# Performance work log

Hardware: AMD Instinct MI355X
Metric: run time of the kernel (lower is better)

Reference implementation:

```python
import jax, jax.numpy as jnp
import numpy as np

D_MODEL = 1024
D_HEAD = 64


def setup_inputs() -> dict:
    key = jax.random.key(0)
    k_x, k_q, k_k, k_v, k_o = jax.random.split(key, 5)
    scale = 1.0 / np.sqrt(D_MODEL)
    residual_stream = jax.random.normal(k_x, (4, 2048, D_MODEL), dtype=jnp.float32)
    Q = scale * jax.random.normal(k_q, (D_MODEL, D_HEAD), dtype=jnp.float32)
    K = scale * jax.random.normal(k_k, (D_MODEL, D_HEAD), dtype=jnp.float32)
    V = scale * jax.random.normal(k_v, (D_MODEL, D_HEAD), dtype=jnp.float32)
    O = scale * jax.random.normal(k_o, (D_MODEL, D_HEAD), dtype=jnp.float32)
    return {"residual_stream": residual_stream, "Q": Q, "K": K, "V": V, "O": O}


def reference(residual_stream, Q, K, V, O) -> jnp.ndarray:
    # queries/keys: [B, S, d_head]
    queries = jnp.einsum('bsd,dh->bsh', residual_stream, Q)
    keys = jnp.einsum('bsd,dh->bsh', residual_stream, K)
    # NOTE: original module applies NO 1/sqrt(d_head) scaling.
    pre_attention = jnp.einsum('bqh,bkh->bqk', queries, keys)  # [B, S, S]
    S = pre_attention.shape[-1]
    causal = jnp.tril(jnp.ones((S, S), dtype=bool))
    pre_attention = jnp.where(causal[None], pre_attention, -jnp.inf)
    attention = jax.nn.softmax(pre_attention, axis=-1)
    # x = residual @ V @ O^T : [B, S, d_model]
    x = jnp.einsum('bsd,dh,eh->bse', residual_stream, V, O)
    return jnp.einsum('bqk,bke->bqe', attention, x)
```

## Files before the change

### kernel.cpp

```cpp
#include <hip/hip_runtime.h>
#include <hip/hip_bf16.h>
#include <math.h>

#define BATCH 4
#define SEQ   2048
#define DM    1024
#define DH    64
#define NROWS (BATCH*SEQ)
#define PVSPLIT 8

typedef __hip_bfloat16 bf16;
typedef __attribute__((ext_vector_type(8))) short short8;
typedef __attribute__((ext_vector_type(8))) unsigned short ushortx8;
typedef __attribute__((ext_vector_type(4))) float floatx4;

__device__ __forceinline__ ushort f2bf(float f) {
    union { bf16 h; ushort u; } cv;
    cv.h = __float2bfloat16(f);
    return cv.u;
}
__device__ __forceinline__ float bf2f(ushort u) {
    union { unsigned int i; float f; } v; v.i = ((unsigned int)u) << 16; return v.f;
}

__device__ __forceinline__ void load_lds16(const ushort* g, ushort* l) {
    __builtin_amdgcn_global_load_lds(
        (const __attribute__((address_space(1))) unsigned int*)g,
        (__attribute__((address_space(3))) unsigned int*)l, 16, 0, 0);
}

__global__ __launch_bounds__(256) void wprep_kernel(
    const float* __restrict__ Q, const float* __restrict__ K,
    const float* __restrict__ V, const float* __restrict__ O,
    ushort* __restrict__ WhT, ushort* __restrict__ WlT,
    ushort* __restrict__ Oh, ushort* __restrict__ Ol)
{
    int n = blockIdx.x;
    if (n < 192) {
        const float* W = (n < 64) ? Q : (n < 128) ? K : V;
        int c = n & 63;
        for (int k = threadIdx.x; k < DM; k += 256) {
            float w = W[k * DH + c];
            ushort hi = f2bf(w);
            WhT[n * DM + k] = hi;
            WlT[n * DM + k] = f2bf(w - bf2f(hi));
        }
    } else {
        int e0 = (n - 192) << 4;
        for (int idx = threadIdx.x; idx < 16 * DH; idx += 256) {
            int off = (e0 << 6) + idx;
            float w = O[off];
            ushort hi = f2bf(w);
            Oh[off] = hi;
            Ol[off] = f2bf(w - bf2f(hi));
        }
    }
}

__global__ __launch_bounds__(256) void qkv_part_kernel(
    const float* __restrict__ x, const ushort* __restrict__ WhT,
    const ushort* __restrict__ WlT, float* __restrict__ Cpart)
{
    __shared__ __align__(16) ushort Xs[2][32][34];
    __shared__ __align__(16) ushort Ws[2][192][34];
    int s0 = blockIdx.x * 32;
    int kb = blockIdx.y * 256;
    int t = threadIdx.x;
    int wave = t >> 6, lane = t & 63, m_ = lane & 15, qd = lane >> 4;
    const floatx4 z4 = {0.f, 0.f, 0.f, 0.f};
    floatx4 accq[2] = {z4, z4}, acck[2] = {z4, z4}, accv[2] = {z4, z4};
    int xr = t >> 3, xc = (t & 7) * 4;
    for (int k0 = 0; k0 < 256; k0 += 32) {
        float4 v = *(const float4*)&x[(size_t)(s0 + xr) * DM + kb + k0 + xc];
        ushort h0 = f2bf(v.x), h1 = f2bf(v.y), h2 = f2bf(v.z), h3 = f2bf(v.w);
        *(ushort4*)&Xs[0][xr][xc] = make_ushort4(h0, h1, h2, h3);
        *(ushort4*)&Xs[1][xr][xc] = make_ushort4(
            f2bf(v.x - bf2f(h0)), f2bf(v.y - bf2f(h1)),
            f2bf(v.z - bf2f(h2)), f2bf(v.w - bf2f(h3)));
        #pragma unroll
        for (int j = 0; j < 3; ++j) {
            int idx = t + j * 256, n = idx >> 2, kc = (idx & 3) * 8;
            *(uint4*)&Ws[0][n][kc] = *(const uint4*)&WhT[n * DM + kb + k0 + kc];
            *(uint4*)&Ws[1][n][kc] = *(const uint4*)&WlT[n * DM + kb + k0 + kc];
        }
        __syncthreads();
        short8 ah[2], al[2];
        #pragma unroll
        for (int mi = 0; mi < 2; ++mi) {
            ah[mi] = *(const short8*)&Xs[0][mi * 16 + m_][qd * 8];
            al[mi] = *(const short8*)&Xs[1][mi * 16 + m_][qd * 8];
        }
        int nq = wave * 16 + m_, nk = 64 + wave * 16 + m_, nv = 128 + wave * 16 + m_;
        short8 bqh = *(const short8*)&Ws[0][nq][qd * 8];
        short8 bql = *(const short8*)&Ws[1][nq][qd * 8];
        short8 bkh = *(const short8*)&Ws[0][nk][qd * 8];
        short8 bkl = *(const short8*)&Ws[1][nk][qd * 8];
        short8 bvh = *(const short8*)&Ws[0][nv][qd * 8];
        #pragma unroll
        for (int mi = 0; mi < 2; ++mi) {
            accq[mi] = __builtin_amdgcn_mfma_f32_16x16x32_bf16(ah[mi], bqh, accq[mi], 0, 0, 0);
            accq[mi] = __builtin_amdgcn_mfma_f32_16x16x32_bf16(al[mi], bqh, accq[mi], 0, 0, 0);
            accq[mi] = __builtin_amdgcn_mfma_f32_16x16x32_bf16(ah[mi], bql, accq[mi], 0, 0, 0);
            acck[mi] = __builtin_amdgcn_mfma_f32_16x16x32_bf16(ah[mi], bkh, acck[mi], 0, 0, 0);
            acck[mi] = __builtin_amdgcn_mfma_f32_16x16x32_bf16(al[mi], bkh, acck[mi], 0, 0, 0);
            acck[mi] = __builtin_amdgcn_mfma_f32_16x16x32_bf16(ah[mi], bkl, acck[mi], 0, 0, 0);
            accv[mi] = __builtin_amdgcn_mfma_f32_16x16x32_bf16(ah[mi], bvh, accv[mi], 0, 0, 0);
        }
        __syncthreads();
    }
    float* Cp = Cpart + (size_t)blockIdx.y * (NROWS * 192);
    #pragma unroll
    for (int mi = 0; mi < 2; ++mi) {
        #pragma unroll
        for (int r = 0; r < 4; ++r) {
            int row = s0 + mi * 16 + qd * 4 + r;
            float* base = Cp + (size_t)row * 192;
            base[wave * 16 + m_]       = accq[mi][r];
            base[64 + wave * 16 + m_]  = acck[mi][r];
            base[128 + wave * 16 + m_] = accv[mi][r];
        }
    }
}

__global__ __launch_bounds__(256) void qkv_reduce_kernel(
    const float* __restrict__ Cpart,
    ushort* __restrict__ qh, ushort* __restrict__ ql,
    ushort* __restrict__ kh, ushort* __restrict__ kl, ushort* __restrict__ xvhT)
{
    __shared__ ushort xvs[32][72];
    const size_t SL = (size_t)NROWS * 192;
    int row0 = blockIdx.x * 32;
    int t = threadIdx.x;
    #pragma unroll
    for (int i = 0; i < 24; ++i) {
        int e = i * 256 + t;
        int r = e / 192, c = e - r * 192;
        size_t row = row0 + r;
        size_t off = row * 192 + c;
        float s = Cpart[off] + Cpart[SL + off] + Cpart[2 * SL + off] + Cpart[3 * SL + off];
        ushort hi = f2bf(s);
        if (c < 64) {
            qh[row * 64 + c] = hi; ql[row * 64 + c] = f2bf(s - bf2f(hi));
        } else if (c < 128) {
            kh[row * 64 + c - 64] = hi; kl[row * 64 + c - 64] = f2bf(s - bf2f(hi));
        } else {
            xvs[r][c - 128] = hi;
        }
    }
    __syncthreads();
    int h = t >> 2, seg = t & 3;
    ushortx8 v;
    #pragma unroll
    for (int k = 0; k < 8; ++k) v[k] = xvs[seg * 8 + k][h];
    int b = row0 >> 11, sl = row0 & 2047;
    *(ushortx8*)&xvhT[(((size_t)(b * 64 + h)) << 11) + sl + seg * 8] = v;
}

__global__ __launch_bounds__(256) void softmax_kernel(
    const ushort* __restrict__ qh, const ushort* __restrict__ ql,
    const ushort* __restrict__ kh, const ushort* __restrict__ kl,
    ushort* __restrict__ P, float* __restrict__ lpart)
{
    __shared__ __align__(16) ushort Qs[2][2][32][72];
    __shared__ float lred[4][2][32];
    int pp = blockIdx.x & 31, b = blockIdx.x >> 5, s = blockIdx.y;
    int jA = pp, jB = 63 - pp;
    int srowA = jA << 5, srowB = jB << 5;
    int s0gA = (b << 11) + srowA, s0gB = (b << 11) + srowB;
    int t = threadIdx.x, wave = t >> 6, lane = t & 63, m_ = lane & 15, qd = lane >> 4;
    #pragma unroll
    for (int i = 0; i < 4; ++i) {
        int idx = i * 256 + t;
        int tile = idx >> 9, hl = (idx >> 8) & 1, r = (idx >> 3) & 31, c = (idx & 7) * 8;
        const ushort* src = (hl ? ql : qh) + (size_t)((tile ? s0gB : s0gA) + r) * 64 + c;
        *(uint4*)&Qs[tile][hl][r][c] = *(const uint4*)src;
    }
    __syncthreads();
    const ushort* khb = kh + ((size_t)b << 11) * 64;
    const ushort* klb = kl + ((size_t)b << 11) * 64;
    int ntA = (jA >> 1) + 1, ntB = (jB >> 1) + 1;
    int nAs = (ntA > s) ? (((ntA - 1 - s) >> 2) + 1) : 0;
    int nBs = (ntB > s) ? (((ntB - 1 - s) >> 2) + 1) : 0;
    int ntot = nAs + nBs;
    const floatx4 z4 = {0.f, 0.f, 0.f, 0.f};
    float llA[2][4] = {{0.f,0.f,0.f,0.f},{0.f,0.f,0.f,0.f}};
    float llB[2][4] = {{0.f,0.f,0.f,0.f},{0.f,0.f,0.f,0.f}};
    for (int it = wave; it < ntot; it += 4) {
        int isA = (it < nAs);
        int ti = isA ? (s + 4 * it) : (s + 4 * (it - nAs));
        int srow = isA ? srowA : srowB;
        int s0g = isA ? s0gA : s0gB;
        int tidx = isA ? 0 : 1;
        int k0 = ti << 6;
        floatx4 acc[2][4];
        #pragma unroll
        for (int mi = 0; mi < 2; ++mi)
            #pragma unroll
            for (int ni = 0; ni < 4; ++ni) acc[mi][ni] = z4;
        #pragma unroll
        for (int kk = 0; kk < 2; ++kk) {
            short8 ah0 = *(const short8*)&Qs[tidx][0][0 * 16 + m_][kk * 32 + qd * 8];
            short8 ah1 = *(const short8*)&Qs[tidx][0][1 * 16 + m_][kk * 32 + qd * 8];
            short8 al0 = *(const short8*)&Qs[tidx][1][0 * 16 + m_][kk * 32 + qd * 8];
            short8 al1 = *(const short8*)&Qs[tidx][1][1 * 16 + m_][kk * 32 + qd * 8];
            #pragma unroll
            for (int ni = 0; ni < 4; ++ni) {
                size_t koff = (size_t)(k0 + ni * 16 + m_) * 64 + kk * 32 + qd * 8;
                short8 bh = *(const short8*)&khb[koff];
                short8 bl = *(const short8*)&klb[koff];
                acc[0][ni] = __builtin_amdgcn_mfma_f32_16x16x32_bf16(ah0, bh, acc[0][ni], 0, 0, 0);
                acc[0][ni] = __builtin_amdgcn_mfma_f32_16x16x32_bf16(al0, bh, acc[0][ni], 0, 0, 0);
                acc[0][ni] = __builtin_amdgcn_mfma_f32_16x16x32_bf16(ah0, bl, acc[0][ni], 0, 0, 0);
                acc[1][ni] = __builtin_amdgcn_mfma_f32_16x16x32_bf16(ah1, bh, acc[1][ni], 0, 0, 0);
                acc[1][ni] = __builtin_amdgcn_mfma_f32_16x16x32_bf16(al1, bh, acc[1][ni], 0, 0, 0);
                acc[1][ni] = __builtin_amdgcn_mfma_f32_16x16x32_bf16(ah1, bl, acc[1][ni], 0, 0, 0);
            }
        }
        #pragma unroll
        for (int mi = 0; mi < 2; ++mi)
            #pragma unroll
            for (int ni = 0; ni < 4; ++ni) {
                int kc = k0 + ni * 16 + m_;
                #pragma unroll
                for (int r = 0; r < 4; ++r) {
                    int row = srow + mi * 16 + qd * 4 + r;
                    float p = (kc <= row) ? __expf(acc[mi][ni][r]) : 0.f;
                    if (isA) llA[mi][r] += p; else llB[mi][r] += p;
                    P[(size_t)(s0g + mi * 16 + qd * 4 + r) * 2048 + kc] = f2bf(p);
                }
            }
    }
    #pragma unroll
    for (int d = 1; d < 16; d <<= 1)
        #pragma unroll
        for (int mi = 0; mi < 2; ++mi)
            #pragma unroll
            for (int r = 0; r < 4; ++r) {
                llA[mi][r] += __shfl_xor(llA[mi][r], d);
                llB[mi][r] += __shfl_xor(llB[mi][r], d);
            }
    if (m_ == 0)
        #pragma unroll
        for (int mi = 0; mi < 2; ++mi)
            #pragma unroll
            for (int r = 0; r < 4; ++r) {
                lred[wave][0][mi * 16 + qd * 4 + r] = llA[mi][r];
                lred[wave][1][mi * 16 + qd * 4 + r] = llB[mi][r];
            }
    __syncthreads();
    if (t < 64) {
        int tile = t >> 5, row = t & 31;
        float sm = lred[0][tile][row] + lred[1][tile][row]
                 + lred[2][tile][row] + lred[3][tile][row];
        lpart[(size_t)s * NROWS + (tile ? s0gB : s0gA) + row] = sm;
    }
}

__global__ __launch_bounds__(256) void pv_kernel(
    const ushort* __restrict__ P, const ushort* __restrict__ xvhT,
    float* __restrict__ AxvPart)
{
    __shared__ __align__(16) ushort AL[2][64 * 64];
    __shared__ __align__(16) ushort AS[2][64 * 64];
    __shared__ __align__(16) ushort Bs[2][64 * 64];
    int bid = blockIdx.x;
    int p = bid >> 5;
    int b = (bid >> 3) & 3;
    int s = bid & 7;
    int m0L = (31 - p) << 6, m0S = p << 6;
    int ntL = 32 - p, ntS = p + 1;
    int nL = (ntL - s + 7) >> 3;
    int nS = (ntS > s) ? ((ntS - s + 7) >> 3) : 0;
    int t = threadIdx.x, wave = t >> 6, lane = t & 63, m_ = lane & 15, qd = lane >> 4;
    const ushort* Pb = P + ((size_t)b << 22);
    const ushort* Xb = xvhT + ((size_t)(b * 64) << 11);
    const floatx4 z4 = {0.f, 0.f, 0.f, 0.f};
    floatx4 accL[2][2], accS[2][2];
    #pragma unroll
    for (int mi = 0; mi < 2; ++mi)
        #pragma unroll
        for (int ni = 0; ni < 2; ++ni) { accL[mi][ni] = z4; accS[mi][ni] = z4; }
    int mb = (wave >> 1) << 5;
    int nb = (wave & 1) << 5;
    int drow = lane >> 3;
    int dlc = ((lane & 7) ^ drow) << 3;
    #define PV_STAGE(tt, buf)                                                    \
        {                                                                        \
            int k0_ = (s + 8 * (tt)) << 6;                                       \
            _Pragma("unroll")                                                    \
            for (int i_ = 0; i_ < 6; ++i_) {                                     \
                int c_ = wave * 6 + i_;                                          \
                if (c_ < 8)                                                      \
                    load_lds16(Pb + (size_t)(m0L + c_ * 8 + drow) * SEQ + k0_ + dlc, \
                               &AL[buf][c_ * 512]);                              \
                else if (c_ < 16)                                                \
                    load_lds16(Xb + (size_t)((c_ - 8) * 8 + drow) * SEQ + k0_ + dlc, \
                               &Bs[buf][(c_ - 8) * 512]);                        \
                else if ((tt) < nS)                                              \
                    load_lds16(Pb + (size_t)(m0S + (c_ - 16) * 8 + drow) * SEQ + k0_ + dlc, \
                               &AS[buf][(c_ - 16) * 512]);                       \
            }                                                                    \
        }
    PV_STAGE(0, 0)
    for (int tt = 0; tt < nL; ++tt) {
        __syncthreads();
        if (tt + 1 < nL) PV_STAGE(tt + 1, (tt + 1) & 1)
        int bufi = tt & 1;
        #pragma unroll
        for (int kk = 0; kk < 2; ++kk) {
            short8 bb[2];
            #pragma unroll
            for (int ni = 0; ni < 2; ++ni) {
                int row = nb + ni * 16 + m_;
                bb[ni] = *(const short8*)&Bs[bufi][row * 64 + (((kk << 2) + qd) ^ (row & 7)) * 8];
            }
            #pragma unroll
            for (int mi = 0; mi < 2; ++mi) {
                int row = mb + mi * 16 + m_;
                short8 aL = *(const short8*)&AL[bufi][row * 64 + (((kk << 2) + qd) ^ (row & 7)) * 8];
                #pragma unroll
                for (int ni = 0; ni < 2; ++ni)
                    accL[mi][ni] = __builtin_amdgcn_mfma_f32_16x16x32_bf16(aL, bb[ni], accL[mi][ni], 0, 0, 0);
            }
            if (tt < nS) {
                #pragma unroll
                for (int mi = 0; mi < 2; ++mi) {
                    int row = mb + mi * 16 + m_;
                    short8 aS = *(const short8*)&AS[bufi][row * 64 + (((kk << 2) + qd) ^ (row & 7)) * 8];
                    #pragma unroll
                    for (int ni = 0; ni < 2; ++ni)
                        accS[mi][ni] = __builtin_amdgcn_mfma_f32_16x16x32_bf16(aS, bb[ni], accS[mi][ni], 0, 0, 0);
                }
            }
        }
    }
    float* Ap = AxvPart + (size_t)s * (NROWS * DH);
    #pragma unroll
    for (int mi = 0; mi < 2; ++mi) {
        #pragma unroll
        for (int r = 0; r < 4; ++r) {
            int rowL = m0L + mb + mi * 16 + qd * 4 + r;
            int rowS = m0S + mb + mi * 16 + qd * 4 + r;
            float* orL = Ap + (size_t)((b << 11) + rowL) * DH + nb;
            float* orS = Ap + (size_t)((b << 11) + rowS) * DH + nb;
            #pragma unroll
            for (int ni = 0; ni < 2; ++ni) {
                orL[ni * 16 + m_] = accL[mi][ni][r];
                orS[ni * 16 + m_] = accS[mi][ni][r];
            }
        }
    }
    #undef PV_STAGE
}

__global__ __launch_bounds__(256) void axv_reduce_kernel(
    const float* __restrict__ AxvPart, const float* __restrict__ lpart,
    ushort* __restrict__ Axvh, ushort* __restrict__ Axvl)
{
    const size_t PSL = (size_t)NROWS * DH;
    int idx = blockIdx.x * 256 + threadIdx.x;
    size_t e = (size_t)idx * 4;
    int r = (int)(e >> 6);
    float4 a = *(const float4*)&AxvPart[e];
    #pragma unroll
    for (int sp = 1; sp < PVSPLIT; ++sp) {
        float4 v = *(const float4*)&AxvPart[sp * PSL + e];
        a.x += v.x; a.y += v.y; a.z += v.z; a.w += v.w;
    }
    float sc = 1.f / (lpart[r] + lpart[NROWS + r]
                    + lpart[2 * NROWS + r] + lpart[3 * NROWS + r]);
    a.x *= sc; a.y *= sc; a.z *= sc; a.w *= sc;
    ushort h0 = f2bf(a.x), h1 = f2bf(a.y), h2 = f2bf(a.z), h3 = f2bf(a.w);
    *(ushort4*)&Axvh[e] = make_ushort4(h0, h1, h2, h3);
    *(ushort4*)&Axvl[e] = make_ushort4(
        f2bf(a.x - bf2f(h0)), f2bf(a.y - bf2f(h1)),
        f2bf(a.z - bf2f(h2)), f2bf(a.w - bf2f(h3)));
}

__global__ __launch_bounds__(256) void out_kernel(
    const ushort* __restrict__ Axvh, const ushort* __restrict__ Axvl,
    const ushort* __restrict__ Oh, const ushort* __restrict__ Ol,
    float* __restrict__ out)
{
    __shared__ __align__(16) ushort As[2][64][72];
    __shared__ __align__(16) ushort Bsh[2][128][72];
    int bid = blockIdx.x;
    int r0 = (bid >> 3) << 6;
    int e0 = (bid & 7) << 7;
    int t = threadIdx.x;
    {
        int tr = t >> 2, tc = (t & 3) << 4;
        const ushort* ah = Axvh + (size_t)(r0 + tr) * DH + tc;
        const ushort* al = Axvl + (size_t)(r0 + tr) * DH + tc;
        *(uint4*)&As[0][tr][tc]     = *(const uint4*)ah;
        *(uint4*)&As[0][tr][tc + 8] = *(const uint4*)(ah + 8);
        *(uint4*)&As[1][tr][tc]     = *(const uint4*)al;
        *(uint4*)&As[1][tr][tc + 8] = *(const uint4*)(al + 8);
    }
    {
        int tr = t >> 1, tc = (t & 1) << 5;
        const ushort* bh = Oh + (size_t)(e0 + tr) * DH + tc;
        const ushort* bl = Ol + (size_t)(e0 + tr) * DH + tc;
        *(uint4*)&Bsh[0][tr][tc]      = *(const uint4*)bh;
        *(uint4*)&Bsh[0][tr][tc + 8]  = *(const uint4*)(bh + 8);
        *(uint4*)&Bsh[0][tr][tc + 16] = *(const uint4*)(bh + 16);
        *(uint4*)&Bsh[0][tr][tc + 24] = *(const uint4*)(bh + 24);
        *(uint4*)&Bsh[1][tr][tc]      = *(const uint4*)bl;
        *(uint4*)&Bsh[1][tr][tc + 8]  = *(const uint4*)(bl + 8);
        *(uint4*)&Bsh[1][tr][tc + 16] = *(const uint4*)(bl + 16);
        *(uint4*)&Bsh[1][tr][tc + 24] = *(const uint4*)(bl + 24);
    }
    __syncthreads();
    int wave = t >> 6, lane = t & 63, m_ = lane & 15, qd = lane >> 4;
    const floatx4 z4 = {0.f, 0.f, 0.f, 0.f};
    floatx4 acc[8] = {z4, z4, z4, z4, z4, z4, z4, z4};
    #pragma unroll
    for (int kk = 0; kk < 2; ++kk) {
        short8 ah = *(const short8*)&As[0][wave * 16 + m_][kk * 32 + qd * 8];
        short8 al = *(const short8*)&As[1][wave * 16 + m_][kk * 32 + qd * 8];
        #pragma unroll
        for (int ni = 0; ni < 8; ++ni) {
            short8 bh = *(const short8*)&Bsh[0][ni * 16 + m_][kk * 32 + qd * 8];
            short8 bl = *(const short8*)&Bsh[1][ni * 16 + m_][kk * 32 + qd * 8];
            acc[ni] = __builtin_amdgcn_mfma_f32_16x16x32_bf16(ah, bh, acc[ni], 0, 0, 0);
            acc[ni] = __builtin_amdgcn_mfma_f32_16x16x32_bf16(al, bh, acc[ni], 0, 0, 0);
            acc[ni] = __builtin_amdgcn_mfma_f32_16x16x32_bf16(ah, bl, acc[ni], 0, 0, 0);
        }
    }
    #pragma unroll
    for (int r = 0; r < 4; ++r) {
        int row = r0 + wave * 16 + qd * 4 + r;
        float* orow = out + (size_t)row * DM + e0;
        #pragma unroll
        for (int ni = 0; ni < 8; ++ni)
            orow[ni * 16 + m_] = acc[ni][r];
    }
}

extern "C" void kernel_launch(void* const* d_in, const int* in_sizes, int n_in,
                              void* d_out, int out_size, void* d_ws, size_t ws_size,
                              hipStream_t stream) {
    const float* x = (const float*)d_in[0];
    const float* Q = (const float*)d_in[1];
    const float* K = (const float*)d_in[2];
    const float* V = (const float*)d_in[3];
    const float* O = (const float*)d_in[4];
    float* out = (float*)d_out;

    char* ws = (char*)d_ws;
    ushort* qh   = (ushort*)(ws);
    ushort* ql   = (ushort*)(ws + (1ull  << 20));
    ushort* kh   = (ushort*)(ws + (2ull  << 20));
    ushort* kl   = (ushort*)(ws + (3ull  << 20));
    ushort* xvhT = (ushort*)(ws + (4ull  << 20));
    ushort* WhT  = (ushort*)(ws + (5ull  << 20));
    ushort* WlT  = (ushort*)(ws + (5ull  << 20) + (512ull << 10));
    float*  lpart = (float*)(ws + (6ull  << 20));
    ushort* Oh   = (ushort*)(ws + (6ull  << 20) + (256ull << 10));
    ushort* Ol   = (ushort*)(ws + (6ull  << 20) + (384ull << 10));
    float*  AxvPart = (float*)(ws + (7ull << 20));
    ushort* Pbuf = (ushort*)(ws + (23ull << 20));
    float*  Cpart = (float*)(ws + (23ull << 20));
    ushort* Axvh = qh;
    ushort* Axvl = ql;

    wprep_kernel<<<256, 256, 0, stream>>>(Q, K, V, O, WhT, WlT, Oh, Ol);
    qkv_part_kernel<<<dim3(NROWS / 32, 4), 256, 0, stream>>>(x, WhT, WlT, Cpart);
    qkv_reduce_kernel<<<NROWS / 32, 256, 0, stream>>>(Cpart, qh, ql, kh, kl, xvhT);
    softmax_kernel<<<dim3(32 * BATCH, 4), 256, 0, stream>>>(qh, ql, kh, kl, Pbuf, lpart);
    pv_kernel<<<16 * 4 * PVSPLIT, 256, 0, stream>>>(Pbuf, xvhT, AxvPart);
    axv_reduce_kernel<<<NROWS * DH / 4 / 256, 256, 0, stream>>>(AxvPart, lpart, Axvh, Axvl);
    out_kernel<<<(NROWS / 64) * 8, 256, 0, stream>>>(Axvh, Axvl, Oh, Ol, out);
}
```

Measured before the change: 162.1 us.

## Fuse softmax and PV into a single flash-style attention kernel

Replaces the separate softmax kernel (which wrote a full bf16 P matrix), the split-K PV kernel and the axv reduction with one attention kernel. It computes S^T tiles via MFMA, exponentiates in registers, and feeds them directly as A operands into the P·XV MFMA, then reduces across waves in LDS. XV is stored in a new packed layout that matches the MFMA operand order. This removes the large P round-trip through global memory and two launches. In exchange, parallelism drops to 256 blocks of 512 threads, and the PV product no longer stages operands through LDS.

```diff
diff --git a/kernel.cpp b/kernel.cpp
--- a/kernel.cpp
+++ b/kernel.cpp
@@ -7,7 +7,6 @@
 #define DM    1024
 #define DH    64
 #define NROWS (BATCH*SEQ)
-#define PVSPLIT 8
 
 typedef __hip_bfloat16 bf16;
 typedef __attribute__((ext_vector_type(8))) short short8;
@@ -21,12 +20,6 @@
 }
 __device__ __forceinline__ float bf2f(ushort u) {
     union { unsigned int i; float f; } v; v.i = ((unsigned int)u) << 16; return v.f;
-}
-
-__device__ __forceinline__ void load_lds16(const ushort* g, ushort* l) {
-    __builtin_amdgcn_global_load_lds(
-        (const __attribute__((address_space(1))) unsigned int*)g,
-        (__attribute__((address_space(3))) unsigned int*)l, 16, 0, 0);
 }
 
 __global__ __launch_bounds__(256) void wprep_kernel(
@@ -125,7 +118,7 @@
 __global__ __launch_bounds__(256) void qkv_reduce_kernel(
     const float* __restrict__ Cpart,
     ushort* __restrict__ qh, ushort* __restrict__ ql,
-    ushort* __restrict__ kh, ushort* __restrict__ kl, ushort* __restrict__ xvhT)
+    ushort* __restrict__ kh, ushort* __restrict__ kl, ushort* __restrict__ xvP)
 {
     __shared__ ushort xvs[32][72];
     const size_t SL = (size_t)NROWS * 192;
@@ -148,233 +141,147 @@
         }
     }
     __syncthreads();
-    int h = t >> 2, seg = t & 3;
+    int h = t & 63, qd = t >> 6;
     ushortx8 v;
     #pragma unroll
-    for (int k = 0; k < 8; ++k) v[k] = xvs[seg * 8 + k][h];
-    int b = row0 >> 11, sl = row0 & 2047;
-    *(ushortx8*)&xvhT[(((size_t)(b * 64 + h)) << 11) + sl + seg * 8] = v;
-}
-
-__global__ __launch_bounds__(256) void softmax_kernel(
+    for (int j = 0; j < 8; ++j)
+        v[j] = xvs[4 * qd + (j & 3) + ((j >> 2) << 4)][h];
+    int b = row0 >> 11, c32 = (row0 & 2047) >> 5;
+    *(ushortx8*)&xvP[((((size_t)b << 6) + c32) * 4 + qd) * 512 + h * 8] = v;
+}
+
+__global__ __launch_bounds__(512) void attn_kernel(
     const ushort* __restrict__ qh, const ushort* __restrict__ ql,
     const ushort* __restrict__ kh, const ushort* __restrict__ kl,
-    ushort* __restrict__ P, float* __restrict__ lpart)
-{
-    __shared__ __align__(16) ushort Qs[2][2][32][72];
-    __shared__ float lred[4][2][32];
-    int pp = blockIdx.x & 31, b = blockIdx.x >> 5, s = blockIdx.y;
-    int jA = pp, jB = 63 - pp;
-    int srowA = jA << 5, srowB = jB << 5;
-    int s0gA = (b << 11) + srowA, s0gB = (b << 11) + srowB;
+    const ushort* __restrict__ xvP,
+    ushort* __restrict__ Axvh, ushort* __restrict__ Axvl)
+{
+    __shared__ __align__(16) ushort Qs[2][2][16][72];
+    __shared__ float LO[2][2][16][68];
+    __shared__ float lred[8][2][16];
+    int pp = blockIdx.x & 63, b = blockIdx.x >> 6;
+    int srowA = pp << 4, srowB = (127 - pp) << 4;
     int t = threadIdx.x, wave = t >> 6, lane = t & 63, m_ = lane & 15, qd = lane >> 4;
-    #pragma unroll
-    for (int i = 0; i < 4; ++i) {
-        int idx = i * 256 + t;
-        int tile = idx >> 9, hl = (idx >> 8) & 1, r = (idx >> 3) & 31, c = (idx & 7) * 8;
-        const ushort* src = (hl ? ql : qh) + (size_t)((tile ? s0gB : s0gA) + r) * 64 + c;
+    {
+        int tile = t >> 8, hl = (t >> 7) & 1, r = (t >> 3) & 15, c = (t & 7) * 8;
+        const ushort* src = (hl ? ql : qh) + (size_t)((b << 11) + (tile ? srowB : srowA) + r) * 64 + c;
         *(uint4*)&Qs[tile][hl][r][c] = *(const uint4*)src;
     }
     __syncthreads();
-    const ushort* khb = kh + ((size_t)b << 11) * 64;
-    const ushort* klb = kl + ((size_t)b << 11) * 64;
-    int ntA = (jA >> 1) + 1, ntB = (jB >> 1) + 1;
-    int nAs = (ntA > s) ? (((ntA - 1 - s) >> 2) + 1) : 0;
-    int nBs = (ntB > s) ? (((ntB - 1 - s) >> 2) + 1) : 0;
-    int ntot = nAs + nBs;
+    int nA = (pp >> 2) + 1, nB = ((127 - pp) >> 2) + 1;
+    int M = nA + nB;
+    const ushort* khb = kh + (((size_t)b << 11)) * 64;
+    const ushort* klb = kl + (((size_t)b << 11)) * 64;
+    const ushort* xvb = xvP + ((size_t)b << 17);
     const floatx4 z4 = {0.f, 0.f, 0.f, 0.f};
-    float llA[2][4] = {{0.f,0.f,0.f,0.f},{0.f,0.f,0.f,0.f}};
-    float llB[2][4] = {{0.f,0.f,0.f,0.f},{0.f,0.f,0.f,0.f}};
-    for (int it = wave; it < ntot; it += 4) {
-        int isA = (it < nAs);
-        int ti = isA ? (s + 4 * it) : (s + 4 * (it - nAs));
-        int srow = isA ? srowA : srowB;
-        int s0g = isA ? s0gA : s0gB;
-        int tidx = isA ? 0 : 1;
-        int k0 = ti << 6;
-        floatx4 acc[2][4];
-        #pragma unroll
-        for (int mi = 0; mi < 2; ++mi)
+    floatx4 accOA[4] = {z4, z4, z4, z4};
+    floatx4 accOB[4] = {z4, z4, z4, z4};
+    float llA = 0.f, llB = 0.f;
+    for (int it = wave; it < M; it += 8) {
+        int tile = (it >= nA);
+        int c = tile ? (it - nA) : it;
+        int srow = tile ? srowB : srowA;
+        int k0 = c << 6;
+        floatx4 accS[4] = {z4, z4, z4, z4};
+        #pragma unroll
+        for (int kk = 0; kk < 2; ++kk) {
+            short8 bqh, bql;
+            if (tile == 0) {
+                bqh = *(const short8*)&Qs[0][0][m_][kk * 32 + qd * 8];
+                bql = *(const short8*)&Qs[0][1][m_][kk * 32 + qd * 8];
+            } else {
+                bqh = *(const short8*)&Qs[1][0][m_][kk * 32 + qd * 8];
+                bql = *(const short8*)&Qs[1][1][m_][kk * 32 + qd * 8];
+            }
             #pragma unroll
-            for (int ni = 0; ni < 4; ++ni) acc[mi][ni] = z4;
-        #pragma unroll
-        for (int kk = 0; kk < 2; ++kk) {
-            short8 ah0 = *(const short8*)&Qs[tidx][0][0 * 16 + m_][kk * 32 + qd * 8];
-            short8 ah1 = *(const short8*)&Qs[tidx][0][1 * 16 + m_][kk * 32 + qd * 8];
-            short8 al0 = *(const short8*)&Qs[tidx][1][0 * 16 + m_][kk * 32 + qd * 8];
-            short8 al1 = *(const short8*)&Qs[tidx][1][1 * 16 + m_][kk * 32 + qd * 8];
+            for (int mt = 0; mt < 4; ++mt) {
+                size_t koff = (size_t)(k0 + mt * 16 + m_) * 64 + kk * 32 + qd * 8;
+                short8 akh = *(const short8*)&khb[koff];
+                short8 akl = *(const short8*)&klb[koff];
+                accS[mt] = __builtin_amdgcn_mfma_f32_16x16x32_bf16(akh, bqh, accS[mt], 0, 0, 0);
+                accS[mt] = __builtin_amdgcn_mfma_f32_16x16x32_bf16(akl, bqh, accS[mt], 0, 0, 0);
+                accS[mt] = __builtin_amdgcn_mfma_f32_16x16x32_bf16(akh, bql, accS[mt], 0, 0, 0);
+            }
+        }
+        int qrow = srow + m_;
+        float lsum = 0.f;
+        short8 pa[2];
+        #pragma unroll
+        for (int h2 = 0; h2 < 2; ++h2) {
             #pragma unroll
-            for (int ni = 0; ni < 4; ++ni) {
-                size_t koff = (size_t)(k0 + ni * 16 + m_) * 64 + kk * 32 + qd * 8;
-                short8 bh = *(const short8*)&khb[koff];
-                short8 bl = *(const short8*)&klb[koff];
-                acc[0][ni] = __builtin_amdgcn_mfma_f32_16x16x32_bf16(ah0, bh, acc[0][ni], 0, 0, 0);
-                acc[0][ni] = __builtin_amdgcn_mfma_f32_16x16x32_bf16(al0, bh, acc[0][ni], 0, 0, 0);
-                acc[0][ni] = __builtin_amdgcn_mfma_f32_16x16x32_bf16(ah0, bl, acc[0][ni], 0, 0, 0);
-                acc[1][ni] = __builtin_amdgcn_mfma_f32_16x16x32_bf16(ah1, bh, acc[1][ni], 0, 0, 0);
-                acc[1][ni] = __builtin_amdgcn_mfma_f32_16x16x32_bf16(al1, bh, acc[1][ni], 0, 0, 0);
-                acc[1][ni] = __builtin_amdgcn_mfma_f32_16x16x32_bf16(ah1, bl, acc[1][ni], 0, 0, 0);
-            }
-        }
-        #pragma unroll
-        for (int mi = 0; mi < 2; ++mi)
-            #pragma unroll
-            for (int ni = 0; ni < 4; ++ni) {
-                int kc = k0 + ni * 16 + m_;
+            for (int tt = 0; tt < 2; ++tt) {
+                int mt = h2 * 2 + tt;
                 #pragma unroll
                 for (int r = 0; r < 4; ++r) {
-                    int row = srow + mi * 16 + qd * 4 + r;
-                    float p = (kc <= row) ? __expf(acc[mi][ni][r]) : 0.f;
-                    if (isA) llA[mi][r] += p; else llB[mi][r] += p;
-                    P[(size_t)(s0g + mi * 16 + qd * 4 + r) * 2048 + kc] = f2bf(p);
+                    int kc = k0 + mt * 16 + qd * 4 + r;
+                    float p = (kc <= qrow) ? __expf(accS[mt][r]) : 0.f;
+                    lsum += p;
+                    pa[h2][tt * 4 + r] = (short)f2bf(p);
                 }
             }
-    }
-    #pragma unroll
-    for (int d = 1; d < 16; d <<= 1)
-        #pragma unroll
-        for (int mi = 0; mi < 2; ++mi)
+        }
+        if (tile == 0) llA += lsum; else llB += lsum;
+        #pragma unroll
+        for (int h2 = 0; h2 < 2; ++h2) {
+            int c32 = (k0 >> 5) + h2;
+            const ushort* xb = xvb + ((size_t)c32 * 4 + qd) * 512 + m_ * 8;
+            short8 x0 = *(const short8*)&xb[0];
+            short8 x1 = *(const short8*)&xb[128];
+            short8 x2 = *(const short8*)&xb[256];
+            short8 x3 = *(const short8*)&xb[384];
+            if (tile == 0) {
+                accOA[0] = __builtin_amdgcn_mfma_f32_16x16x32_bf16(pa[h2], x0, accOA[0], 0, 0, 0);
+                accOA[1] = __builtin_amdgcn_mfma_f32_16x16x32_bf16(pa[h2], x1, accOA[1], 0, 0, 0);
+                accOA[2] = __builtin_amdgcn_mfma_f32_16x16x32_bf16(pa[h2], x2, accOA[2], 0, 0, 0);
+                accOA[3] = __builtin_amdgcn_mfma_f32_16x16x32_bf16(pa[h2], x3, accOA[3], 0, 0, 0);
+            } else {
+                accOB[0] = __builtin_amdgcn_mfma_f32_16x16x32_bf16(pa[h2], x0, accOB[0], 0, 0, 0);
+                accOB[1] = __builtin_amdgcn_mfma_f32_16x16x32_bf16(pa[h2], x1, accOB[1], 0, 0, 0);
+                accOB[2] = __builtin_amdgcn_mfma_f32_16x16x32_bf16(pa[h2], x2, accOB[2], 0, 0, 0);
+                accOB[3] = __builtin_amdgcn_mfma_f32_16x16x32_bf16(pa[h2], x3, accOB[3], 0, 0, 0);
+            }
+        }
+    }
+    llA += __shfl_xor(llA, 16); llA += __shfl_xor(llA, 32);
+    llB += __shfl_xor(llB, 16); llB += __shfl_xor(llB, 32);
+    if (qd == 0) { lred[wave][0][m_] = llA; lred[wave][1][m_] = llB; }
+    int part = wave >> 2, w4 = wave & 3;
+    for (int w = 0; w < 4; ++w) {
+        if (w4 == w) {
             #pragma unroll
-            for (int r = 0; r < 4; ++r) {
-                llA[mi][r] += __shfl_xor(llA[mi][r], d);
-                llB[mi][r] += __shfl_xor(llB[mi][r], d);
-            }
-    if (m_ == 0)
-        #pragma unroll
-        for (int mi = 0; mi < 2; ++mi)
-            #pragma unroll
-            for (int r = 0; r < 4; ++r) {
-                lred[wave][0][mi * 16 + qd * 4 + r] = llA[mi][r];
-                lred[wave][1][mi * 16 + qd * 4 + r] = llB[mi][r];
-            }
-    __syncthreads();
-    if (t < 64) {
-        int tile = t >> 5, row = t & 31;
-        float sm = lred[0][tile][row] + lred[1][tile][row]
-                 + lred[2][tile][row] + lred[3][tile][row];
-        lpart[(size_t)s * NROWS + (tile ? s0gB : s0gA) + row] = sm;
-    }
-}
-
-__global__ __launch_bounds__(256) void pv_kernel(
-    const ushort* __restrict__ P, const ushort* __restrict__ xvhT,
-    float* __restrict__ AxvPart)
-{
-    __shared__ __align__(16) ushort AL[2][64 * 64];
-    __shared__ __align__(16) ushort AS[2][64 * 64];
-    __shared__ __align__(16) ushort Bs[2][64 * 64];
-    int bid = blockIdx.x;
-    int p = bid >> 5;
-    int b = (bid >> 3) & 3;
-    int s = bid & 7;
-    int m0L = (31 - p) << 6, m0S = p << 6;
-    int ntL = 32 - p, ntS = p + 1;
-    int nL = (ntL - s + 7) >> 3;
-    int nS = (ntS > s) ? ((ntS - s + 7) >> 3) : 0;
-    int t = threadIdx.x, wave = t >> 6, lane = t & 63, m_ = lane & 15, qd = lane >> 4;
-    const ushort* Pb = P + ((size_t)b << 22);
-    const ushort* Xb = xvhT + ((size_t)(b * 64) << 11);
-    const floatx4 z4 = {0.f, 0.f, 0.f, 0.f};
-    floatx4 accL[2][2], accS[2][2];
-    #pragma unroll
-    for (int mi = 0; mi < 2; ++mi)
-        #pragma unroll
-        for (int ni = 0; ni < 2; ++ni) { accL[mi][ni] = z4; accS[mi][ni] = z4; }
-    int mb = (wave >> 1) << 5;
-    int nb = (wave & 1) << 5;
-    int drow = lane >> 3;
-    int dlc = ((lane & 7) ^ drow) << 3;
-    #define PV_STAGE(tt, buf)                                                    \
-        {                                                                        \
-            int k0_ = (s + 8 * (tt)) << 6;                                       \
-            _Pragma("unroll")                                                    \
-            for (int i_ = 0; i_ < 6; ++i_) {                                     \
-                int c_ = wave * 6 + i_;                                          \
-                if (c_ < 8)                                                      \
-                    load_lds16(Pb + (size_t)(m0L + c_ * 8 + drow) * SEQ + k0_ + dlc, \
-                               &AL[buf][c_ * 512]);                              \
-                else if (c_ < 16)                                                \
-                    load_lds16(Xb + (size_t)((c_ - 8) * 8 + drow) * SEQ + k0_ + dlc, \
-                               &Bs[buf][(c_ - 8) * 512]);                        \
-                else if ((tt) < nS)                                              \
-                    load_lds16(Pb + (size_t)(m0S + (c_ - 16) * 8 + drow) * SEQ + k0_ + dlc, \
-                               &AS[buf][(c_ - 16) * 512]);                       \
-            }                                                                    \
-        }
-    PV_STAGE(0, 0)
-    for (int tt = 0; tt < nL; ++tt) {
+            for (int hn = 0; hn < 4; ++hn)
+                #pragma unroll
+                for (int r = 0; r < 4; ++r) {
+                    int q = qd * 4 + r, h = hn * 16 + m_;
+                    if (w == 0) {
+                        LO[part][0][q][h] = accOA[hn][r];
+                        LO[part][1][q][h] = accOB[hn][r];
+                    } else {
+                        LO[part][0][q][h] += accOA[hn][r];
+                        LO[part][1][q][h] += accOB[hn][r];
+                    }
+                }
+        }
         __syncthreads();
-        if (tt + 1 < nL) PV_STAGE(tt + 1, (tt + 1) & 1)
-        int bufi = tt & 1;
-        #pragma unroll
-        for (int kk = 0; kk < 2; ++kk) {
-            short8 bb[2];
-            #pragma unroll
-            for (int ni = 0; ni < 2; ++ni) {
-                int row = nb + ni * 16 + m_;
-                bb[ni] = *(const short8*)&Bs[bufi][row * 64 + (((kk << 2) + qd) ^ (row & 7)) * 8];
-            }
-            #pragma unroll
-            for (int mi = 0; mi < 2; ++mi) {
-                int row = mb + mi * 16 + m_;
-                short8 aL = *(const short8*)&AL[bufi][row * 64 + (((kk << 2) + qd) ^ (row & 7)) * 8];
-                #pragma unroll
-                for (int ni = 0; ni < 2; ++ni)
-                    accL[mi][ni] = __builtin_amdgcn_mfma_f32_16x16x32_bf16(aL, bb[ni], accL[mi][ni], 0, 0, 0);
-            }
-            if (tt < nS) {
-                #pragma unroll
-                for (int mi = 0; mi < 2; ++mi) {
-                    int row = mb + mi * 16 + m_;
-                    short8 aS = *(const short8*)&AS[bufi][row * 64 + (((kk << 2) + qd) ^ (row & 7)) * 8];
-                    #pragma unroll
-                    for (int ni = 0; ni < 2; ++ni)
-                        accS[mi][ni] = __builtin_amdgcn_mfma_f32_16x16x32_bf16(aS, bb[ni], accS[mi][ni], 0, 0, 0);
-                }
-            }
-        }
-    }
-    float* Ap = AxvPart + (size_t)s * (NROWS * DH);
-    #pragma unroll
-    for (int mi = 0; mi < 2; ++mi) {
-        #pragma unroll
-        for (int r = 0; r < 4; ++r) {
-            int rowL = m0L + mb + mi * 16 + qd * 4 + r;
-            int rowS = m0S + mb + mi * 16 + qd * 4 + r;
-            float* orL = Ap + (size_t)((b << 11) + rowL) * DH + nb;
-            float* orS = Ap + (size_t)((b << 11) + rowS) * DH + nb;
-            #pragma unroll
-            for (int ni = 0; ni < 2; ++ni) {
-                orL[ni * 16 + m_] = accL[mi][ni][r];
-                orS[ni * 16 + m_] = accS[mi][ni][r];
-            }
-        }
-    }
-    #undef PV_STAGE
-}
-
-__global__ __launch_bounds__(256) void axv_reduce_kernel(
-    const float* __restrict__ AxvPart, const float* __restrict__ lpart,
-    ushort* __restrict__ Axvh, ushort* __restrict__ Axvl)
-{
-    const size_t PSL = (size_t)NROWS * DH;
-    int idx = blockIdx.x * 256 + threadIdx.x;
-    size_t e = (size_t)idx * 4;
-    int r = (int)(e >> 6);
-    float4 a = *(const float4*)&AxvPart[e];
-    #pragma unroll
-    for (int sp = 1; sp < PVSPLIT; ++sp) {
-        float4 v = *(const float4*)&AxvPart[sp * PSL + e];
-        a.x += v.x; a.y += v.y; a.z += v.z; a.w += v.w;
-    }
-    float sc = 1.f / (lpart[r] + lpart[NROWS + r]
-                    + lpart[2 * NROWS + r] + lpart[3 * NROWS + r]);
-    a.x *= sc; a.y *= sc; a.z *= sc; a.w *= sc;
-    ushort h0 = f2bf(a.x), h1 = f2bf(a.y), h2 = f2bf(a.z), h3 = f2bf(a.w);
-    *(ushort4*)&Axvh[e] = make_ushort4(h0, h1, h2, h3);
-    *(ushort4*)&Axvl[e] = make_ushort4(
-        f2bf(a.x - bf2f(h0)), f2bf(a.y - bf2f(h1)),
-        f2bf(a.z - bf2f(h2)), f2bf(a.w - bf2f(h3)));
+    }
+    int tile2 = t >> 8, qq = (t >> 4) & 15, h0 = (t & 15) * 4;
+    int srow2 = tile2 ? srowB : srowA;
+    float lt = 0.f;
+    #pragma unroll
+    for (int w = 0; w < 8; ++w) lt += lred[w][tile2][qq];
+    float sc = 1.f / lt;
+    ushort4 hv, lv;
+    float v0 = (LO[0][tile2][qq][h0 + 0] + LO[1][tile2][qq][h0 + 0]) * sc;
+    float v1 = (LO[0][tile2][qq][h0 + 1] + LO[1][tile2][qq][h0 + 1]) * sc;
+    float v2 = (LO[0][tile2][qq][h0 + 2] + LO[1][tile2][qq][h0 + 2]) * sc;
+    float v3 = (LO[0][tile2][qq][h0 + 3] + LO[1][tile2][qq][h0 + 3]) * sc;
+    hv.x = f2bf(v0); lv.x = f2bf(v0 - bf2f(hv.x));
+    hv.y = f2bf(v1); lv.y = f2bf(v1 - bf2f(hv.y));
+    hv.z = f2bf(v2); lv.z = f2bf(v2 - bf2f(hv.z));
+    hv.w = f2bf(v3); lv.w = f2bf(v3 - bf2f(hv.w));
+    size_t orow = (size_t)((b << 11) + srow2 + qq) * 64 + h0;
+    *(ushort4*)&Axvh[orow] = hv;
+    *(ushort4*)&Axvl[orow] = lv;
 }
 
 __global__ __launch_bounds__(256) void out_kernel(
@@ -452,23 +359,18 @@
     ushort* ql   = (ushort*)(ws + (1ull  << 20));
     ushort* kh   = (ushort*)(ws + (2ull  << 20));
     ushort* kl   = (ushort*)(ws + (3ull  << 20));
-    ushort* xvhT = (ushort*)(ws + (4ull  << 20));
+    ushort* xvP  = (ushort*)(ws + (4ull  << 20));
     ushort* WhT  = (ushort*)(ws + (5ull  << 20));
     ushort* WlT  = (ushort*)(ws + (5ull  << 20) + (512ull << 10));
-    float*  lpart = (float*)(ws + (6ull  << 20));
-    ushort* Oh   = (ushort*)(ws + (6ull  << 20) + (256ull << 10));
-    ushort* Ol   = (ushort*)(ws + (6ull  << 20) + (384ull << 10));
-    float*  AxvPart = (float*)(ws + (7ull << 20));
-    ushort* Pbuf = (ushort*)(ws + (23ull << 20));
+    ushort* Oh   = (ushort*)(ws + (6ull  << 20));
+    ushort* Ol   = (ushort*)(ws + (6ull  << 20) + (128ull << 10));
+    ushort* Axvh = (ushort*)(ws + (7ull  << 20));
+    ushort* Axvl = (ushort*)(ws + (8ull  << 20));
     float*  Cpart = (float*)(ws + (23ull << 20));
-    ushort* Axvh = qh;
-    ushort* Axvl = ql;
 
     wprep_kernel<<<256, 256, 0, stream>>>(Q, K, V, O, WhT, WlT, Oh, Ol);
     qkv_part_kernel<<<dim3(NROWS / 32, 4), 256, 0, stream>>>(x, WhT, WlT, Cpart);
-    qkv_reduce_kernel<<<NROWS / 32, 256, 0, stream>>>(Cpart, qh, ql, kh, kl, xvhT);
-    softmax_kernel<<<dim3(32 * BATCH, 4), 256, 0, stream>>>(qh, ql, kh, kl, Pbuf, lpart);
-    pv_kernel<<<16 * 4 * PVSPLIT, 256, 0, stream>>>(Pbuf, xvhT, AxvPart);
-    axv_reduce_kernel<<<NROWS * DH / 4 / 256, 256, 0, stream>>>(AxvPart, lpart, Axvh, Axvl);
+    qkv_reduce_kernel<<<NROWS / 32, 256, 0, stream>>>(Cpart, qh, ql, kh, kl, xvP);
+    attn_kernel<<<64 * BATCH, 512, 0, stream>>>(qh, ql, kh, kl, xvP, Axvh, Axvl);
     out_kernel<<<(NROWS / 64) * 8, 256, 0, stream>>>(Axvh, Axvl, Oh, Ol, out);
 }
```

Measured after the change: 152.7 us. -5.7%, faster.
